# Optimization experiments

Hardware: AMD Instinct MI355X
Metric: run time of the kernel (lower is better)

The kernel has to match this reference:

```python
import jax, jax.numpy as jnp
import numpy as np

B, N, D = 1, 4096, 3072
H, DH = 16, 64
INNER = H * DH  # 1024
SCALE = DH ** -0.5
EPS = 1e-5


def setup_inputs() -> dict:
    key = jax.random.key(0)
    ks = jax.random.split(key, 4)
    x = jax.random.normal(ks[0], (B, N, D), jnp.float32)
    pe = jax.random.normal(ks[1], (1, 1, N, DH // 2, 2, 2), jnp.float32)
    w_qkv = jax.random.normal(ks[2], (3 * INNER, D), jnp.float32) * 0.02
    w_out = jax.random.normal(ks[3], (D, INNER), jnp.float32) * 0.02
    ln_g = jnp.ones((D,), jnp.float32)
    ln_b = jnp.zeros((D,), jnp.float32)
    return {"x": x, "pe": pe, "w_qkv": w_qkv, "w_out": w_out, "ln_g": ln_g, "ln_b": ln_b}


def _apply_rope(t, pe):
    # t: [b,h,n,d], pe: [1,1,n,d/2,2,2] (Flux rope layout)
    b, h, n, d = t.shape
    t_ = t.reshape(b, h, n, d // 2, 1, 2)
    out = pe[..., 0] * t_[..., 0] + pe[..., 1] * t_[..., 1]  # [b,h,n,d/2,2]
    return out.reshape(b, h, n, d)


def reference(x, pe, w_qkv, w_out, ln_g, ln_b):
    # LayerNorm (norm2)
    mu = jnp.mean(x, axis=-1, keepdims=True)
    var = jnp.mean((x - mu) ** 2, axis=-1, keepdims=True)
    xn = (x - mu) / jnp.sqrt(var + EPS) * ln_g + ln_b
    # QKV projection (no bias)
    qkv = xn @ w_qkv.T  # [b,n,3*inner]
    q, k, v = jnp.split(qkv, 3, axis=-1)
    def split_heads(t):
        return t.reshape(B, N, H, DH).transpose(0, 2, 1, 3)  # b h n d
    q, k, v = split_heads(q), split_heads(k), split_heads(v)
    # RoPE on q and k (attention_aug_bbox with mask=None, aug idx = -1 -> plain rope attn)
    q = _apply_rope(q, pe)
    k = _apply_rope(k, pe)
    scores = jnp.einsum('bhqd,bhkd->bhqk', q, k) * SCALE
    attn = jax.nn.softmax(scores, axis=-1)
    o = jnp.einsum('bhqk,bhkd->bhqd', attn, v)
    o = o.transpose(0, 2, 1, 3).reshape(B, N, INNER)  # b n (h d)
    return o @ w_out.T  # [b,n,dim]
```

## Files before the change

kernel.cpp:

```cpp
#include <hip/hip_runtime.h>
#include <hip/hip_bf16.h>

typedef unsigned short u16;
typedef __attribute__((ext_vector_type(8))) short bf16x8;
typedef __attribute__((ext_vector_type(4))) float f32x4;

#define N_TOK 4096
#define DMODEL 3072
#define NH 16
#define DHEAD 64
#define INNER 1024
#define SCALE_LOG2E 0.18033688011112042f

__device__ __forceinline__ u16 f2bf(float f) {
    union { float f; unsigned u; } un; un.f = f;
    unsigned r = un.u + 0x7fffu + ((un.u >> 16) & 1u);
    return (u16)(r >> 16);
}
__device__ __forceinline__ float bf2f(u16 u) {
    union { unsigned u; float f; } x; x.u = ((unsigned)u) << 16; return x.f;
}
__device__ __forceinline__ unsigned pk2bf(float a, float b) {
    union { float f; unsigned u; } ua, ub; ua.f = a; ub.f = b;
    return __builtin_amdgcn_perm(ub.u + 0x8000u, ua.u + 0x8000u, 0x07060302u);
}
__device__ __forceinline__ void load_lds16(const u16* g, u16* l) {
    __builtin_amdgcn_global_load_lds(
        (const __attribute__((address_space(1))) unsigned int*)g,
        (__attribute__((address_space(3))) unsigned int*)l, 16, 0, 0);
}

__device__ __forceinline__ bf16x8 build_bp(unsigned u0, unsigned u1,
                                           unsigned w0, unsigned w1) {
    auto a = __builtin_amdgcn_permlane32_swap(u0, w0, false, false);
    auto b = __builtin_amdgcn_permlane16_swap(a[0], a[1], false, false);
    auto c = __builtin_amdgcn_permlane32_swap(u1, w1, false, false);
    auto d = __builtin_amdgcn_permlane16_swap(c[0], c[1], false, false);
    union { unsigned w[4]; bf16x8 v; } r;
    r.w[0] = b[0]; r.w[1] = d[0]; r.w[2] = b[1]; r.w[3] = d[1];
    return r.v;
}

__global__ __launch_bounds__(256) void prep(const float* __restrict__ x,
                                            const float* __restrict__ g,
                                            const float* __restrict__ b,
                                            u16* __restrict__ xn,
                                            const float* __restrict__ w_qkv,
                                            u16* __restrict__ wq,
                                            const float* __restrict__ w_out,
                                            u16* __restrict__ wo) {
    int bid = blockIdx.x;
    int tid = threadIdx.x;
    if (bid < 4096) {
        int row = bid;
        const float4* xr = (const float4*)(x + (size_t)row * DMODEL);
        float4 v[3];
        float s = 0.f, ss = 0.f;
#pragma unroll
        for (int i = 0; i < 3; ++i) {
            v[i] = xr[i * 256 + tid];
            s  += v[i].x + v[i].y + v[i].z + v[i].w;
            ss += v[i].x * v[i].x + v[i].y * v[i].y + v[i].z * v[i].z + v[i].w * v[i].w;
        }
#pragma unroll
        for (int off = 32; off; off >>= 1) {
            s  += __shfl_xor(s, off);
            ss += __shfl_xor(ss, off);
        }
        __shared__ float red[8];
        int wid = tid >> 6, lane = tid & 63;
        if (lane == 0) { red[wid] = s; red[wid + 4] = ss; }
        __syncthreads();
        s  = red[0] + red[1] + red[2] + red[3];
        ss = red[4] + red[5] + red[6] + red[7];
        float mean = s * (1.f / DMODEL);
        float var  = ss * (1.f / DMODEL) - mean * mean;
        float rstd = rsqrtf(var + 1e-5f);
        ushort4* orow = (ushort4*)(xn + (size_t)row * DMODEL);
#pragma unroll
        for (int i = 0; i < 3; ++i) {
            float4 gg = ((const float4*)g)[i * 256 + tid];
            float4 bb = ((const float4*)b)[i * 256 + tid];
            ushort4 o;
            o.x = f2bf((v[i].x - mean) * rstd * gg.x + bb.x);
            o.y = f2bf((v[i].y - mean) * rstd * gg.y + bb.y);
            o.z = f2bf((v[i].z - mean) * rstd * gg.z + bb.z);
            o.w = f2bf((v[i].w - mean) * rstd * gg.w + bb.w);
            orow[i * 256 + tid] = o;
        }
    } else if (bid < 4096 + 2048) {
        const int n4 = 3 * INNER * DMODEL / 4;
        for (int i = (bid - 4096) * 256 + tid; i < n4; i += 2048 * 256) {
            float4 v = ((const float4*)w_qkv)[i];
            ushort4 o;
            o.x = f2bf(v.x); o.y = f2bf(v.y); o.z = f2bf(v.z); o.w = f2bf(v.w);
            ((ushort4*)wq)[i] = o;
        }
    } else {
        const int n4 = DMODEL * INNER / 4;
        for (int i = (bid - 6144) * 256 + tid; i < n4; i += 512 * 256) {
            float4 v = ((const float4*)w_out)[i];
            ushort4 o;
            o.x = f2bf(v.x); o.y = f2bf(v.y); o.z = f2bf(v.z); o.w = f2bf(v.w);
            ((ushort4*)wo)[i] = o;
        }
    }
}


#define VM5 asm volatile("s_waitcnt vmcnt(5)" ::: "memory")
#define VM4 asm volatile("s_waitcnt vmcnt(4)" ::: "memory")
#define VM3 asm volatile("s_waitcnt vmcnt(3)" ::: "memory")
#define VM0 asm volatile("s_waitcnt vmcnt(0)" ::: "memory")
#define LGK8 asm volatile("s_waitcnt lgkmcnt(8)" ::: "memory")
#define NOPS ((void)0)

#define ST_A(d, h, t) do { \
    load_lds16(pA##h##0 + (size_t)(t) * 64, &lds[(d) * 16384 + (h) * 8192 + dq]); \
    load_lds16(pA##h##1 + (size_t)(t) * 64, &lds[(d) * 16384 + (h) * 8192 + dq + 512]); \
  } while (0)
#define ST_B1(d, u, t) \
    load_lds16(pB##u + (size_t)(t) * 64, &lds[32768 + (d) * 12288 + (u) * 4096 + wid * 512])

#define PHASE(d, p, STAGE, PRE, POST) do { \
    bf16x8 afr[2][2]; \
    if ((p) == 0) { \
      _Pragma("unroll") for (int nf = 0; nf < 3; ++nf) { \
        bfr[nf][0] = *(const bf16x8*)&lds[32768 + (d) * 12288 + baseB + nf * 1024 + c0]; \
        bfr[nf][1] = *(const bf16x8*)&lds[32768 + (d) * 12288 + baseB + nf * 1024 + c1]; \
      } \
    } \
    _Pragma("unroll") for (int mfl = 0; mfl < 2; ++mfl) { \
      afr[mfl][0] = *(const bf16x8*)&lds[(d) * 16384 + (p) * 4096 + mfl * 1024 + baseA + c0]; \
      afr[mfl][1] = *(const bf16x8*)&lds[(d) * 16384 + (p) * 4096 + mfl * 1024 + baseA + c1]; \
    } \
    STAGE; \
    PRE; \
    __builtin_amdgcn_s_barrier(); \
    asm volatile("s_waitcnt lgkmcnt(0)" ::: "memory"); \
    __builtin_amdgcn_sched_barrier(0); \
    __builtin_amdgcn_s_setprio(1); \
    _Pragma("unroll") for (int mfl = 0; mfl < 2; ++mfl) \
      _Pragma("unroll") for (int nf = 0; nf < 3; ++nf) { \
        acc[(p) * 2 + mfl][nf] = __builtin_amdgcn_mfma_f32_16x16x32_bf16(afr[mfl][0], bfr[nf][0], acc[(p) * 2 + mfl][nf], 0, 0, 0); \
        acc[(p) * 2 + mfl][nf] = __builtin_amdgcn_mfma_f32_16x16x32_bf16(afr[mfl][1], bfr[nf][1], acc[(p) * 2 + mfl][nf], 0, 0, 0); \
      } \
    __builtin_amdgcn_s_setprio(0); \
    POST; \
    __builtin_amdgcn_s_barrier(); \
  } while (0)

template <int MODE>
__global__ __launch_bounds__(512, 2) void gemm256(const u16* __restrict__ A,
                                                  const u16* __restrict__ B,
                                                  void* __restrict__ C,
                                                  int M, int Nn, int K,
                                                  const float* __restrict__ pe,
                                                  u16* __restrict__ Qr,
                                                  u16* __restrict__ Kr,
                                                  u16* __restrict__ Vt) {
    __shared__ u16 lds[57344];
    const int tid = threadIdx.x;
    const int lane = tid & 63, wid = tid >> 6;
    const int wm = wid >> 2, wn = wid & 3;
    const int l15 = lane & 15, quad = lane >> 4;
    const int sw = l15 & 7;

    int nbx = Nn / 192;
    int cpx = gridDim.x >> 3;
    int wg = (blockIdx.x & 7) * cpx + (blockIdx.x >> 3);
    int m0 = (wg / nbx) << 8, n0 = (wg % nbx) * 192;

    const int baseA = wm * 2048 + l15 * 64;
    const int baseB = wn * 3072 + l15 * 64;
    const int c0 = (quad ^ sw) * 8;
    const int c1 = ((4 + quad) ^ sw) * 8;
    const int dq = wid * 1024;

    const u16 *pA00, *pA01, *pA10, *pA11, *pB0, *pB1, *pB2;
    {
        int scol = ((lane & 7) ^ (lane >> 3)) * 8;
#define MKSRCA(h, j, PA) { \
        int ell = (h) * 128 + (wid * 2 + (j)) * 8 + (lane >> 3); \
        int g = ell >> 6, wmh = (ell >> 5) & 1, r = ell & 31; \
        PA = A + (size_t)(m0 + wmh * 128 + g * 32 + r) * K + scol; }
#define MKSRCB(u, PB) { \
        int ell = (u) * 64 + wid * 8 + (lane >> 3); \
        PB = B + (size_t)(n0 + ell) * K + scol; }
        MKSRCA(0, 0, pA00) MKSRCA(0, 1, pA01)
        MKSRCA(1, 0, pA10) MKSRCA(1, 1, pA11)
        MKSRCB(0, pB0) MKSRCB(1, pB1) MKSRCB(2, pB2)
#undef MKSRCA
#undef MKSRCB
    }

    f32x4 acc[8][3];
    f32x4 zero4 = {0.f, 0.f, 0.f, 0.f};
#pragma unroll
    for (int i = 0; i < 8; ++i)
#pragma unroll
        for (int j = 0; j < 3; ++j) acc[i][j] = zero4;
    bf16x8 bfr[3][2];

    ST_B1(0, 0, 0); ST_B1(0, 1, 0); ST_B1(0, 2, 0); ST_A(0, 0, 0); ST_A(0, 1, 0);
    ST_B1(1, 0, 1); ST_B1(1, 1, 1); ST_B1(1, 2, 1); ST_A(1, 0, 1);
    VM5;
    __builtin_amdgcn_s_barrier();

    const int NIT = (K >> 7) - 1;
    for (int i = 0; i < NIT; ++i) {
        int t = 2 * i;
        PHASE(0, 0, ST_A(1, 1, t + 1), LGK8, NOPS);
        PHASE(0, 1, ST_B1(0, 0, t + 2), NOPS, NOPS);
        PHASE(0, 2, ST_B1(0, 1, t + 2), NOPS, NOPS);
        PHASE(0, 3, ST_B1(0, 2, t + 2), NOPS, VM3);
        PHASE(1, 0, ST_A(0, 0, t + 2), LGK8, NOPS);
        PHASE(1, 1, ST_A(0, 1, t + 2), NOPS, NOPS);
        PHASE(1, 2, ST_B1(1, 0, t + 3), NOPS, NOPS);
        PHASE(1, 3, { ST_B1(1, 1, t + 3); ST_B1(1, 2, t + 3); ST_A(1, 0, t + 3); }, NOPS, VM5);
    }
    {
        int T = K >> 6;
        PHASE(0, 0, ST_A(1, 1, T - 1), LGK8, NOPS);
        PHASE(0, 1, NOPS, NOPS, NOPS);
        PHASE(0, 2, NOPS, NOPS, NOPS);
        PHASE(0, 3, NOPS, NOPS, VM0);
        PHASE(1, 0, NOPS, LGK8, NOPS);
        PHASE(1, 1, NOPS, NOPS, NOPS);
        PHASE(1, 2, NOPS, NOPS, NOPS);
        PHASE(1, 3, NOPS, NOPS, NOPS);
    }

    if (MODE == 0) {
#pragma unroll
        for (int mf = 0; mf < 8; ++mf)
#pragma unroll
            for (int nf = 0; nf < 3; ++nf)
#pragma unroll
                for (int r = 0; r < 4; ++r) {
                    int rr = m0 + wm * 128 + mf * 16 + quad * 4 + r;
                    int cc = n0 + wn * 48 + nf * 16 + l15;
                    ((float*)C)[(size_t)rr * Nn + cc] = acc[mf][nf][r];
                }
    } else {
#pragma unroll
        for (int nf = 0; nf < 3; ++nf) {
            int cc = n0 + wn * 48 + nf * 16 + l15;
            if (cc < 2048) {
                const int isQ = (cc < 1024);
                const float scl = isQ ? SCALE_LOG2E : 1.f;
                u16* dst = isQ ? Qr : Kr;
                int hh = (cc & 1023) >> 6;
                int ii = (cc & 63) >> 1;
                int jj = cc & 1;
#pragma unroll
                for (int mf = 0; mf < 8; ++mf)
#pragma unroll
                    for (int r = 0; r < 4; ++r) {
                        int rr = m0 + wm * 128 + mf * 16 + quad * 4 + r;
                        float v = acc[mf][nf][r];
                        float vp = __shfl_xor(v, 1);
                        float v0 = jj ? vp : v;
                        float v1 = jj ? v : vp;
                        const float* pw = pe + (size_t)rr * 128 + ii * 4 + jj * 2;
                        float ov = (pw[0] * v0 + pw[1] * v1) * scl;
                        dst[((size_t)hh * N_TOK + rr) * 64 + (cc & 63)] = f2bf(ov);
                    }
            } else {
                int hh = (cc - 2048) >> 6, dd = cc & 63;
#pragma unroll
                for (int mf = 0; mf < 8; ++mf) {
                    int rr = m0 + wm * 128 + mf * 16 + quad * 4;
                    ushort4 o4;
                    o4.x = f2bf(acc[mf][nf][0]); o4.y = f2bf(acc[mf][nf][1]);
                    o4.z = f2bf(acc[mf][nf][2]); o4.w = f2bf(acc[mf][nf][3]);
                    *(ushort4*)&Vt[((size_t)hh * 64 + dd) * N_TOK + rr] = o4;
                }
            }
        }
    }
}


#define FA_STAGE3(dst, kt) do { \
    load_lds16(&Kh[(size_t)((kt) + krow) * DHEAD + csw], &lds_all[(dst) + kbase]); \
    load_lds16(&Kh[(size_t)((kt) + krow + 8) * DHEAD + csw], &lds_all[(dst) + kbase + 512]); \
    load_lds16(&Vh[(size_t)krow * N_TOK + (kt) + csw], &lds_all[(dst) + 4096 + kbase]); \
    load_lds16(&Vh[(size_t)(krow + 8) * N_TOK + (kt) + csw], &lds_all[(dst) + 4096 + kbase + 512]); \
  } while (0)

#define FA_READ(CUR, AV) do { \
    _Pragma("unroll") for (int tt = 0; tt < 4; ++tt) \
      _Pragma("unroll") for (int kc = 0; kc < 2; ++kc) \
        bk[tt][kc] = *(const bf16x8*)&lds_all[(CUR) + (tt * 16 + l15) * 64 + (((kc * 4 + quad) ^ sw) * 8)]; \
    __builtin_amdgcn_sched_barrier(0); \
    _Pragma("unroll") for (int tt = 0; tt < 4; ++tt) \
      _Pragma("unroll") for (int kc = 0; kc < 2; ++kc) \
        AV[tt][kc] = *(const bf16x8*)&lds_all[(CUR) + 4096 + (tt * 16 + l15) * 64 + (((kc * 4 + quad) ^ sw) * 8)]; \
    __builtin_amdgcn_sched_barrier(0); \
  } while (0)

#define LGK8F do { asm volatile("s_waitcnt lgkmcnt(8)" ::: "memory"); __builtin_amdgcn_sched_barrier(0); } while (0)
#define LGK0F do { asm volatile("s_waitcnt lgkmcnt(0)" ::: "memory"); __builtin_amdgcn_sched_barrier(0); } while (0)

#define FA_QK(S) do { \
    __builtin_amdgcn_s_setprio(1); \
    _Pragma("unroll") for (int mtQ = 0; mtQ < 2; ++mtQ) \
      _Pragma("unroll") for (int ntK = 0; ntK < 4; ++ntK) { \
        f32x4 t0 = __builtin_amdgcn_mfma_f32_16x16x32_bf16(bk[ntK][0], aq[mtQ][0], zero4, 0, 0, 0); \
        S[mtQ][ntK] = __builtin_amdgcn_mfma_f32_16x16x32_bf16(bk[ntK][1], aq[mtQ][1], t0, 0, 0, 0); \
      } \
    __builtin_amdgcn_s_setprio(0); \
  } while (0)

#define FA_SMPV(SP, AVP) do { \
    _Pragma("unroll") for (int mtQ = 0; mtQ < 2; ++mtQ) { \
      unsigned pw[4][2]; \
      _Pragma("unroll") for (int ntK = 0; ntK < 4; ++ntK) { \
        float e0 = __builtin_amdgcn_exp2f(SP[mtQ][ntK][0]); \
        float e1 = __builtin_amdgcn_exp2f(SP[mtQ][ntK][1]); \
        float e2 = __builtin_amdgcn_exp2f(SP[mtQ][ntK][2]); \
        float e3 = __builtin_amdgcn_exp2f(SP[mtQ][ntK][3]); \
        asm("v_cvt_pk_bf16_f32 %0, %1, %2" : "=v"(pw[ntK][0]) : "v"(e0), "v"(e1)); \
        asm("v_cvt_pk_bf16_f32 %0, %1, %2" : "=v"(pw[ntK][1]) : "v"(e2), "v"(e3)); \
      } \
      bf16x8 bp0 = build_bp(pw[0][0], pw[0][1], pw[1][0], pw[1][1]); \
      bf16x8 bp1 = build_bp(pw[2][0], pw[2][1], pw[3][0], pw[3][1]); \
      __builtin_amdgcn_s_setprio(1); \
      lacc[mtQ] = __builtin_amdgcn_mfma_f32_16x16x32_bf16(ones, bp0, lacc[mtQ], 0, 0, 0); \
      lacc[mtQ] = __builtin_amdgcn_mfma_f32_16x16x32_bf16(ones, bp1, lacc[mtQ], 0, 0, 0); \
      _Pragma("unroll") for (int dt = 0; dt < 4; ++dt) { \
        o[mtQ][dt] = __builtin_amdgcn_mfma_f32_16x16x32_bf16(AVP[dt][0], bp0, o[mtQ][dt], 0, 0, 0); \
        o[mtQ][dt] = __builtin_amdgcn_mfma_f32_16x16x32_bf16(AVP[dt][1], bp1, o[mtQ][dt], 0, 0, 0); \
      } \
      __builtin_amdgcn_s_setprio(0); \
    } \
  } while (0)

__global__ __launch_bounds__(256, 2) void flash_attn(const u16* __restrict__ Q,
                                                     const u16* __restrict__ K,
                                                     const u16* __restrict__ Vt,
                                                     u16* __restrict__ O) {
    __shared__ u16 lds_all[24576];
    int tid = threadIdx.x, lane = tid & 63, wid = tid >> 6;
    int l15 = lane & 15, quad = lane >> 4;
    int sw = l15 & 7;
    int h = blockIdx.y;
    int q0 = blockIdx.x * 128 + wid * 32;
    const u16* Qh = Q + (size_t)h * N_TOK * DHEAD;
    const u16* Kh = K + (size_t)h * N_TOK * DHEAD;
    const u16* Vh = Vt + (size_t)h * DHEAD * N_TOK;

    f32x4 zero4 = {0.f, 0.f, 0.f, 0.f};
    bf16x8 ones;
#pragma unroll
    for (int i = 0; i < 8; ++i) ones[i] = (short)0x3F80;

    bf16x8 aq[2][2];
#pragma unroll
    for (int mtQ = 0; mtQ < 2; ++mtQ)
#pragma unroll
        for (int kc = 0; kc < 2; ++kc)
            aq[mtQ][kc] = *(const bf16x8*)&Qh[(size_t)(q0 + mtQ * 16 + l15) * DHEAD + kc * 32 + quad * 8];

    f32x4 o[2][4], lacc[2];
#pragma unroll
    for (int mtQ = 0; mtQ < 2; ++mtQ) {
#pragma unroll
        for (int dt = 0; dt < 4; ++dt) o[mtQ][dt] = zero4;
        lacc[mtQ] = zero4;
    }

    int rowoff = lane >> 3;
    int krow = wid * 16 + rowoff;
    int kbase = wid * 1024;
    int csw = ((lane & 7) ^ rowoff) * 8;

    bf16x8 bk[4][2], avA[4][2], avB[4][2];
    f32x4 sA[2][4], sB[2][4];

    FA_STAGE3(0, 0);
    FA_STAGE3(8192, 64);
    VM4;
    __builtin_amdgcn_s_barrier();
    __builtin_amdgcn_sched_barrier(0);

    FA_READ(0, avA);
    FA_STAGE3(16384, 128);
    LGK8F;
    FA_QK(sA);
    LGK0F;
    VM4;
    __builtin_amdgcn_s_barrier();
    __builtin_amdgcn_sched_barrier(0);

    int cur = 8192;
    for (int i = 0; i < 31; ++i) {
        int tB = 2 * i + 1, tA = 2 * i + 2;
        FA_READ(cur, avB);
        { int stg = cur + 16384; if (stg >= 24576) stg -= 24576;
          FA_STAGE3(stg, (tB + 2) * 64); }
        LGK8F;
        FA_QK(sB);
        FA_SMPV(sA, avA);
        LGK0F;
        VM4;
        __builtin_amdgcn_s_barrier();
        __builtin_amdgcn_sched_barrier(0);
        cur += 8192; if (cur >= 24576) cur -= 24576;
        FA_READ(cur, avA);
        if (tA + 2 < 64) { int stg = cur + 16384; if (stg >= 24576) stg -= 24576;
                           FA_STAGE3(stg, (tA + 2) * 64); }
        LGK8F;
        FA_QK(sA);
        FA_SMPV(sB, avB);
        LGK0F;
        if (tA + 2 < 64) { VM4; } else { VM0; }
        __builtin_amdgcn_s_barrier();
        __builtin_amdgcn_sched_barrier(0);
        cur += 8192; if (cur >= 24576) cur -= 24576;
    }
    FA_READ(cur, avB);
    LGK8F;
    FA_QK(sB);
    FA_SMPV(sA, avA);
    LGK0F;
    FA_SMPV(sB, avB);

    __syncthreads();
    u16* scratch = lds_all + wid * 2048;
#pragma unroll
    for (int mtQ = 0; mtQ < 2; ++mtQ) {
        float rl = 1.f / lacc[mtQ][0];
#pragma unroll
        for (int dt = 0; dt < 4; ++dt) {
            uint2 ov;
            ov.x = pk2bf(o[mtQ][dt][0] * rl, o[mtQ][dt][1] * rl);
            ov.y = pk2bf(o[mtQ][dt][2] * rl, o[mtQ][dt][3] * rl);
            *(uint2*)&scratch[(mtQ * 16 + l15) * 64 + dt * 16 + quad * 4] = ov;
        }
    }
    __syncthreads();
#pragma unroll
    for (int p = 0; p < 4; ++p) {
        int q_local = p * 8 + (lane >> 3);
        int dcol = (lane & 7) * 8;
        bf16x8 v = *(const bf16x8*)&scratch[q_local * 64 + dcol];
        *(bf16x8*)&O[(size_t)(q0 + q_local) * INNER + h * 64 + dcol] = v;
    }
}

extern "C" void kernel_launch(void* const* d_in, const int* in_sizes, int n_in,
                              void* d_out, int out_size, void* d_ws, size_t ws_size,
                              hipStream_t stream) {
    const float* x     = (const float*)d_in[0];
    const float* pe    = (const float*)d_in[1];
    const float* w_qkv = (const float*)d_in[2];
    const float* w_out = (const float*)d_in[3];
    const float* ln_g  = (const float*)d_in[4];
    const float* ln_b  = (const float*)d_in[5];
    float* out = (float*)d_out;

    char* ws = (char*)d_ws;
    u16* xn  = (u16*)ws;  ws += (size_t)N_TOK * DMODEL * 2;
    u16* wq  = (u16*)ws;  ws += (size_t)3 * INNER * DMODEL * 2;
    u16* wo  = (u16*)ws;  ws += (size_t)DMODEL * INNER * 2;
    u16* Qr  = (u16*)ws;  ws += (size_t)NH * N_TOK * DHEAD * 2;
    u16* Kr  = (u16*)ws;  ws += (size_t)NH * N_TOK * DHEAD * 2;
    u16* Vt  = (u16*)ws;  ws += (size_t)NH * DHEAD * N_TOK * 2;
    u16* Ob  = (u16*)ws;  ws += (size_t)N_TOK * INNER * 2;

    prep<<<4096 + 2048 + 512, 256, 0, stream>>>(x, ln_g, ln_b, xn, w_qkv, wq, w_out, wo);
    gemm256<2><<<dim3((N_TOK / 256) * (DMODEL / 192)), 512, 0, stream>>>(
        xn, wq, nullptr, N_TOK, DMODEL, DMODEL, pe, Qr, Kr, Vt);
    flash_attn<<<dim3(N_TOK / 128, NH), 256, 0, stream>>>(Qr, Kr, Vt, Ob);
    gemm256<0><<<dim3((N_TOK / 256) * (DMODEL / 192)), 512, 0, stream>>>(
        Ob, wo, out, N_TOK, DMODEL, INNER, nullptr, nullptr, nullptr, nullptr);
}
```

Measured before the change: 331.1 us.

## Fuse QKV GEMM, flash attention and output GEMM into one cooperative kernel

Merges the QKV projection GEMM, flash attention and output projection into a single persistent cooperative kernel of 256 blocks of 512 threads, separated by grid-wide syncs. Flash attention is recast to 8 waves per block covering 256 queries, with each wave staging half as many K/V rows per tile. The aim is to remove launch gaps and tail effects between the three kernels. The cost is two grid barriers and a change in occupancy for the attention phase. Block mapping is hardcoded to 256 blocks, which matches 16x16 GEMM tiles and 16 heads times 16 query tiles.

```diff
diff --git a/kernel.cpp b/kernel.cpp
--- a/kernel.cpp
+++ b/kernel.cpp
@@ -1,5 +1,8 @@
 #include <hip/hip_runtime.h>
 #include <hip/hip_bf16.h>
+#include <hip/hip_cooperative_groups.h>
+
+namespace cg = cooperative_groups;
 
 typedef unsigned short u16;
 typedef __attribute__((ext_vector_type(8))) short bf16x8;
@@ -109,8 +112,8 @@
 
 
 #define VM5 asm volatile("s_waitcnt vmcnt(5)" ::: "memory")
-#define VM4 asm volatile("s_waitcnt vmcnt(4)" ::: "memory")
 #define VM3 asm volatile("s_waitcnt vmcnt(3)" ::: "memory")
+#define VM2 asm volatile("s_waitcnt vmcnt(2)" ::: "memory")
 #define VM0 asm volatile("s_waitcnt vmcnt(0)" ::: "memory")
 #define LGK8 asm volatile("s_waitcnt lgkmcnt(8)" ::: "memory")
 #define NOPS ((void)0)
@@ -151,15 +154,11 @@
   } while (0)
 
 template <int MODE>
-__global__ __launch_bounds__(512, 2) void gemm256(const u16* __restrict__ A,
-                                                  const u16* __restrict__ B,
-                                                  void* __restrict__ C,
-                                                  int M, int Nn, int K,
-                                                  const float* __restrict__ pe,
-                                                  u16* __restrict__ Qr,
-                                                  u16* __restrict__ Kr,
-                                                  u16* __restrict__ Vt) {
-    __shared__ u16 lds[57344];
+__device__ void gemm_body(const u16* __restrict__ A, const u16* __restrict__ B,
+                          void* __restrict__ C, int M, int Nn, int K,
+                          const float* __restrict__ pe, u16* __restrict__ Qr,
+                          u16* __restrict__ Kr, u16* __restrict__ Vt,
+                          u16* lds, int bid) {
     const int tid = threadIdx.x;
     const int lane = tid & 63, wid = tid >> 6;
     const int wm = wid >> 2, wn = wid & 3;
@@ -167,8 +166,7 @@
     const int sw = l15 & 7;
 
     int nbx = Nn / 192;
-    int cpx = gridDim.x >> 3;
-    int wg = (blockIdx.x & 7) * cpx + (blockIdx.x >> 3);
+    int wg = (bid & 7) * 32 + (bid >> 3);
     int m0 = (wg / nbx) << 8, n0 = (wg % nbx) * 192;
 
     const int baseA = wm * 2048 + l15 * 64;
@@ -282,11 +280,9 @@
 }
 
 
-#define FA_STAGE3(dst, kt) do { \
+#define FA_STAGE2(dst, kt) do { \
     load_lds16(&Kh[(size_t)((kt) + krow) * DHEAD + csw], &lds_all[(dst) + kbase]); \
-    load_lds16(&Kh[(size_t)((kt) + krow + 8) * DHEAD + csw], &lds_all[(dst) + kbase + 512]); \
     load_lds16(&Vh[(size_t)krow * N_TOK + (kt) + csw], &lds_all[(dst) + 4096 + kbase]); \
-    load_lds16(&Vh[(size_t)(krow + 8) * N_TOK + (kt) + csw], &lds_all[(dst) + 4096 + kbase + 512]); \
   } while (0)
 
 #define FA_READ(CUR, AV) do { \
@@ -337,16 +333,14 @@
     } \
   } while (0)
 
-__global__ __launch_bounds__(256, 2) void flash_attn(const u16* __restrict__ Q,
-                                                     const u16* __restrict__ K,
-                                                     const u16* __restrict__ Vt,
-                                                     u16* __restrict__ O) {
-    __shared__ u16 lds_all[24576];
+__device__ void flash_body(const u16* __restrict__ Q, const u16* __restrict__ K,
+                           const u16* __restrict__ Vt, u16* __restrict__ O,
+                           u16* lds_all, int bid) {
     int tid = threadIdx.x, lane = tid & 63, wid = tid >> 6;
     int l15 = lane & 15, quad = lane >> 4;
     int sw = l15 & 7;
-    int h = blockIdx.y;
-    int q0 = blockIdx.x * 128 + wid * 32;
+    int h = bid >> 4;
+    int q0 = (bid & 15) * 256 + wid * 32;
     const u16* Qh = Q + (size_t)h * N_TOK * DHEAD;
     const u16* Kh = K + (size_t)h * N_TOK * DHEAD;
     const u16* Vh = Vt + (size_t)h * DHEAD * N_TOK;
@@ -372,25 +366,25 @@
     }
 
     int rowoff = lane >> 3;
-    int krow = wid * 16 + rowoff;
-    int kbase = wid * 1024;
+    int krow = wid * 8 + rowoff;
+    int kbase = wid * 512;
     int csw = ((lane & 7) ^ rowoff) * 8;
 
     bf16x8 bk[4][2], avA[4][2], avB[4][2];
     f32x4 sA[2][4], sB[2][4];
 
-    FA_STAGE3(0, 0);
-    FA_STAGE3(8192, 64);
-    VM4;
+    FA_STAGE2(0, 0);
+    FA_STAGE2(8192, 64);
+    VM2;
     __builtin_amdgcn_s_barrier();
     __builtin_amdgcn_sched_barrier(0);
 
     FA_READ(0, avA);
-    FA_STAGE3(16384, 128);
+    FA_STAGE2(16384, 128);
     LGK8F;
     FA_QK(sA);
     LGK0F;
-    VM4;
+    VM2;
     __builtin_amdgcn_s_barrier();
     __builtin_amdgcn_sched_barrier(0);
 
@@ -399,23 +393,23 @@
         int tB = 2 * i + 1, tA = 2 * i + 2;
         FA_READ(cur, avB);
         { int stg = cur + 16384; if (stg >= 24576) stg -= 24576;
-          FA_STAGE3(stg, (tB + 2) * 64); }
+          FA_STAGE2(stg, (tB + 2) * 64); }
         LGK8F;
         FA_QK(sB);
         FA_SMPV(sA, avA);
         LGK0F;
-        VM4;
+        VM2;
         __builtin_amdgcn_s_barrier();
         __builtin_amdgcn_sched_barrier(0);
         cur += 8192; if (cur >= 24576) cur -= 24576;
         FA_READ(cur, avA);
         if (tA + 2 < 64) { int stg = cur + 16384; if (stg >= 24576) stg -= 24576;
-                           FA_STAGE3(stg, (tA + 2) * 64); }
+                           FA_STAGE2(stg, (tA + 2) * 64); }
         LGK8F;
         FA_QK(sA);
         FA_SMPV(sB, avB);
         LGK0F;
-        if (tA + 2 < 64) { VM4; } else { VM0; }
+        if (tA + 2 < 64) { VM2; } else { VM0; }
         __builtin_amdgcn_s_barrier();
         __builtin_amdgcn_sched_barrier(0);
         cur += 8192; if (cur >= 24576) cur -= 24576;
@@ -448,6 +442,24 @@
         bf16x8 v = *(const bf16x8*)&scratch[q_local * 64 + dcol];
         *(bf16x8*)&O[(size_t)(q0 + q_local) * INNER + h * 64 + dcol] = v;
     }
+}
+
+__global__ __launch_bounds__(512, 2) void mega(const u16* __restrict__ xn,
+                                               const u16* __restrict__ wq,
+                                               const u16* __restrict__ wo,
+                                               const float* __restrict__ pe,
+                                               u16* __restrict__ Qr,
+                                               u16* __restrict__ Kr,
+                                               u16* __restrict__ Vt,
+                                               u16* __restrict__ Ob,
+                                               float* __restrict__ out) {
+    __shared__ u16 lds[57344];
+    int bid = blockIdx.x;
+    gemm_body<2>(xn, wq, nullptr, N_TOK, DMODEL, DMODEL, pe, Qr, Kr, Vt, lds, bid);
+    cg::this_grid().sync();
+    flash_body(Qr, Kr, Vt, Ob, lds, bid);
+    cg::this_grid().sync();
+    gemm_body<0>(Ob, wo, out, N_TOK, DMODEL, INNER, nullptr, nullptr, nullptr, nullptr, lds, bid);
 }
 
 extern "C" void kernel_launch(void* const* d_in, const int* in_sizes, int n_in,
@@ -471,9 +483,8 @@
     u16* Ob  = (u16*)ws;  ws += (size_t)N_TOK * INNER * 2;
 
     prep<<<4096 + 2048 + 512, 256, 0, stream>>>(x, ln_g, ln_b, xn, w_qkv, wq, w_out, wo);
-    gemm256<2><<<dim3((N_TOK / 256) * (DMODEL / 192)), 512, 0, stream>>>(
-        xn, wq, nullptr, N_TOK, DMODEL, DMODEL, pe, Qr, Kr, Vt);
-    flash_attn<<<dim3(N_TOK / 128, NH), 256, 0, stream>>>(Qr, Kr, Vt, Ob);
-    gemm256<0><<<dim3((N_TOK / 256) * (DMODEL / 192)), 512, 0, stream>>>(
-        Ob, wo, out, N_TOK, DMODEL, INNER, nullptr, nullptr, nullptr, nullptr);
-}
+
+    void* args[] = {(void*)&xn, (void*)&wq, (void*)&wo, (void*)&pe,
+                    (void*)&Qr, (void*)&Kr, (void*)&Vt, (void*)&Ob, (void*)&out};
+    hipLaunchCooperativeKernel((const void*)mega, dim3(256), dim3(512), args, 0, stream);
+}
```

Result: slower. 439.0 us (+32.6%).
